# Kernel tuning notes

Measured on AMD Instinct MI355X. Metric: run time of the kernel, lower is better.

## Reference

```python
import jax, jax.numpy as jnp
import numpy as np

B, S, D = 8, 2048, 512


def setup_inputs() -> dict:
    key = jax.random.key(0)
    ks = jax.random.split(key, 8)
    x = jax.random.normal(ks[0], (B, S, D), dtype=jnp.float32)
    mask = jax.random.randint(ks[1], (B, S, 1), 0, 2, dtype=jnp.int32)
    Wq = jax.random.normal(ks[2], (D, D), dtype=jnp.float32) / np.sqrt(D)
    bq = jax.random.normal(ks[3], (D,), dtype=jnp.float32) * 0.01
    Wk = jax.random.normal(ks[4], (D, D), dtype=jnp.float32) / np.sqrt(D)
    bk = jax.random.normal(ks[5], (D,), dtype=jnp.float32) * 0.01
    Wv = jax.random.normal(ks[6], (D, D), dtype=jnp.float32) / np.sqrt(D)
    bv = jax.random.normal(ks[7], (D,), dtype=jnp.float32) * 0.01
    return {"x": x, "mask": mask, "Wq": Wq, "bq": bq, "Wk": Wk, "bk": bk, "Wv": Wv, "bv": bv}


def reference(x, mask, Wq, bq, Wk, bk, Wv, bv):
    # torch Linear: y = x @ W^T + b
    Q = jnp.einsum('bsd,ed->bse', x, Wq) + bq
    K = jnp.einsum('bsd,ed->bse', x, Wk) + bk
    V = jnp.einsum('bsd,ed->bse', x, Wv) + bv
    scale = 1.0 / jnp.sqrt(jnp.asarray(x.shape[-1], dtype=x.dtype))
    scores = jnp.einsum('bqd,bkd->bqk', Q, K) * scale  # [B, S, S]
    attn_mask = jnp.transpose(mask, (0, 2, 1))  # [B, 1, S], broadcasts over queries
    scores = jnp.where(attn_mask == 0, jnp.asarray(-10000.0, dtype=scores.dtype), scores)
    attn = jax.nn.softmax(scores, axis=-1)
    return jnp.einsum('bqk,bkd->bqd', attn, V)
```

## Files before the change

### kernel.cpp

```cpp
#include <hip/hip_runtime.h>
#include <cstddef>

#define BB 8
#define SS 2048
#define DD 512
#define MM (BB * SS)

typedef __attribute__((ext_vector_type(8))) short bf16x8;
typedef __attribute__((ext_vector_type(4))) float f32x4;
typedef __attribute__((ext_vector_type(4))) unsigned short u16x4;

__device__ __forceinline__ f32x4 mfma16(bf16x8 a, bf16x8 b, f32x4 c) {
  return __builtin_amdgcn_mfma_f32_16x16x32_bf16(a, b, c, 0, 0, 0);
}
__device__ __forceinline__ unsigned short f2bf(float f) {
  unsigned int u = __float_as_uint(f);
  u += 0x7fffu + ((u >> 16) & 1u);
  return (unsigned short)(u >> 16);
}
__device__ __forceinline__ void gld16(const void* g, void* l) {
  __builtin_amdgcn_global_load_lds((const __attribute__((address_space(1))) void*)g,
                                   (__attribute__((address_space(3))) void*)l, 16, 0, 0);
}

__global__ void cvt_bf16_kernel(const float* __restrict__ in,
                                unsigned short* __restrict__ out, int n4) {
  int i = blockIdx.x * blockDim.x + threadIdx.x;
  if (i >= n4) return;
  f32x4 v = reinterpret_cast<const f32x4*>(in)[i];
  u16x4 o;
  o[0] = f2bf(v[0]);
  o[1] = f2bf(v[1]);
  o[2] = f2bf(v[2]);
  o[3] = f2bf(v[3]);
  reinterpret_cast<u16x4*>(out)[i] = o;
}
__global__ void cvt_w3_kernel(const float* __restrict__ s0, const float* __restrict__ s1,
                              const float* __restrict__ s2, unsigned short* __restrict__ d0,
                              unsigned short* __restrict__ d1, unsigned short* __restrict__ d2) {
  const float* s = blockIdx.y == 0 ? s0 : (blockIdx.y == 1 ? s1 : s2);
  unsigned short* d = blockIdx.y == 0 ? d0 : (blockIdx.y == 1 ? d1 : d2);
  int i = blockIdx.x * blockDim.x + threadIdx.x;
  f32x4 v = reinterpret_cast<const f32x4*>(s)[i];
  u16x4 o;
  o[0] = f2bf(v[0]);
  o[1] = f2bf(v[1]);
  o[2] = f2bf(v[2]);
  o[3] = f2bf(v[3]);
  reinterpret_cast<u16x4*>(d)[i] = o;
}

__global__ void mask_scan_kernel(const int* __restrict__ mask, int* __restrict__ idx,
                                 int* __restrict__ nbArr) {
  __shared__ int part[256];
  const int b = blockIdx.x;
  const int t = threadIdx.x;
  int m[8], c = 0;
#pragma unroll
  for (int e = 0; e < 8; ++e) {
    m[e] = mask[b * SS + t * 8 + e];
    c += (m[e] != 0);
  }
  int v = c;
  part[t] = v;
  __syncthreads();
  for (int off = 1; off < 256; off <<= 1) {
    int u = (t >= off) ? part[t - off] : 0;
    __syncthreads();
    v += u;
    part[t] = v;
    __syncthreads();
  }
  int base = v - c;
#pragma unroll
  for (int e = 0; e < 8; ++e)
    if (m[e]) idx[b * SS + base++] = t * 8 + e;
  const int nb = part[255];
  if (t == 255) nbArr[b] = nb;
  for (int j = nb + t; j < SS; j += 256) idx[b * SS + j] = 0;
}

__global__ __launch_bounds__(256, 2) void qkv_gemm_kernel(
    const unsigned short* __restrict__ X, const unsigned short* __restrict__ W0,
    const unsigned short* __restrict__ W1, const unsigned short* __restrict__ W2,
    const float* __restrict__ b0, const float* __restrict__ b1,
    const float* __restrict__ b2, unsigned short* __restrict__ O0,
    unsigned short* __restrict__ O1, unsigned short* __restrict__ O2) {
  __shared__ unsigned char a_lds[128 * 128];
  __shared__ unsigned char b_lds[128 * 128];
  const int tid = threadIdx.x;
  const int w = tid >> 6, l = tid & 63, lr = l & 15, hi = l >> 4;
  const int which = blockIdx.y >> 2;
  const unsigned short* W = which == 0 ? W0 : (which == 1 ? W1 : W2);
  const float* bias = which == 0 ? b0 : (which == 1 ? b1 : b2);
  unsigned short* out = which == 0 ? O0 : (which == 1 ? O1 : O2);
  const int m0 = blockIdx.x * 128;
  const int n0 = (blockIdx.y & 3) * 128;
  const int wm = (w >> 1) * 64, wn = (w & 1) * 64;
  const int srow = l >> 3, gchunk = (l & 7) ^ (srow & 7);

  f32x4 acc[4][4];
#pragma unroll
  for (int mt = 0; mt < 4; ++mt)
#pragma unroll
    for (int nt = 0; nt < 4; ++nt) acc[mt][nt] = (f32x4){0.f, 0.f, 0.f, 0.f};

  const unsigned short* ga = X + (size_t)(m0 + w * 32 + srow) * DD + gchunk * 8;
  const unsigned short* gb = W + (size_t)(n0 + w * 32 + srow) * DD + gchunk * 8;

  for (int k0 = 0; k0 < DD; k0 += 64) {
#pragma unroll
    for (int ii = 0; ii < 4; ++ii) {
      gld16(ga + (size_t)ii * 8 * DD + k0, &a_lds[(w * 4 + ii) * 1024]);
      gld16(gb + (size_t)ii * 8 * DD + k0, &b_lds[(w * 4 + ii) * 1024]);
    }
    __syncthreads();
#pragma unroll
    for (int dkl = 0; dkl < 2; ++dkl) {
      const int gc = dkl * 4 + hi;
      bf16x8 af[4], bfr[4];
#pragma unroll
      for (int mt = 0; mt < 4; ++mt) {
        const int row = wm + mt * 16 + lr;
        af[mt] = *reinterpret_cast<const bf16x8*>(
            &a_lds[row * 128 + ((gc ^ (row & 7)) * 16)]);
      }
#pragma unroll
      for (int nt = 0; nt < 4; ++nt) {
        const int row = wn + nt * 16 + lr;
        bfr[nt] = *reinterpret_cast<const bf16x8*>(
            &b_lds[row * 128 + ((gc ^ (row & 7)) * 16)]);
      }
#pragma unroll
      for (int mt = 0; mt < 4; ++mt)
#pragma unroll
        for (int nt = 0; nt < 4; ++nt)
          acc[mt][nt] = mfma16(af[mt], bfr[nt], acc[mt][nt]);
    }
    __syncthreads();
  }

#pragma unroll
  for (int nt = 0; nt < 4; ++nt) {
    const int col = n0 + wn + nt * 16 + lr;
    const float bv = bias[col];
#pragma unroll
    for (int mt = 0; mt < 4; ++mt)
#pragma unroll
      for (int r = 0; r < 4; ++r) {
        const int row = m0 + wm + mt * 16 + hi * 4 + r;
        out[(size_t)row * DD + col] = f2bf(acc[mt][nt][r] + bv);
      }
  }
}

__global__ void vtrans_kernel(const unsigned short* __restrict__ V,
                              const int* __restrict__ idx, const int* __restrict__ nbArr,
                              unsigned short* __restrict__ VT2) {
  __shared__ unsigned short t[64][72];
  const int b = blockIdx.z;
  const int kt = blockIdx.x;
  const int d0 = blockIdx.y * 64;
  const int tid = threadIdx.x;
  const int c = tid & 63, rg = tid >> 6;
  const int nb = nbArr[b];
#pragma unroll
  for (int i = 0; i < 16; ++i) {
    const int row = rg * 16 + i;
    const int s = kt * 64 + row;
    const int src = s < nb ? idx[b * SS + s] : 0;
    t[row][c] = V[((size_t)b * SS + src) * DD + d0 + c];
  }
  __syncthreads();
#pragma unroll
  for (int i = 0; i < 16; ++i) {
    const int ix = i * 256 + tid;
    const int jj = ix & 7;
    const int dl = (ix >> 3) & 63;
    const int cc = ix >> 9;
    VT2[(((size_t)(b * 32 + kt) * 8 + cc) * 512 + d0 + dl) * 8 + jj] =
        t[cc * 8 + jj][dl];
  }
}

__global__ __launch_bounds__(256, 2) void attn_kernel(
    const unsigned short* __restrict__ Q, const unsigned short* __restrict__ K,
    const unsigned short* __restrict__ VT2, const int* __restrict__ idx,
    const int* __restrict__ nbArr, float* __restrict__ Out,
    float* __restrict__ Apart, float* __restrict__ mlpart) {
  __shared__ unsigned char k_lds[32 * 1024];
  __shared__ unsigned char vt_lds[4 * 512 * 16];
  __shared__ unsigned short pbuf[4][16][32];
  const int tid = threadIdx.x;
  const int w = tid >> 6, l = tid & 63, lr = l & 15, hi = l >> 4;
  const int bid = blockIdx.x;
  const int b = bid & 7;
  const int qt = (bid >> 3) >> 1;
  const int sp = (bid >> 3) & 1;
  const int q0 = qt * 64 + w * 16;
  const float scale = 0.044194173824159216f;

  const int nb = nbArr[b];
  const int ntile = (nb + 31) >> 5;
  const int half = (ntile + 1) >> 1;
  const int lo = sp == 0 ? 0 : half;
  const int hi_t = sp == 0 ? half : ntile;

  const unsigned short* __restrict__ Qb = Q + (size_t)b * SS * DD;
  const unsigned short* __restrict__ Kb = K + (size_t)b * SS * DD;
  const unsigned short* __restrict__ Vb = VT2 + (size_t)b * SS * DD;
  const int* __restrict__ idxb = idx + b * SS;

  bf16x8 qf[16];
#pragma unroll
  for (int dk = 0; dk < 16; ++dk)
    qf[dk] = *reinterpret_cast<const bf16x8*>(
        &Qb[(size_t)(q0 + lr) * DD + dk * 32 + hi * 8]);

  f32x4 oacc[32];
#pragma unroll
  for (int i = 0; i < 32; ++i) oacc[i] = (f32x4){0.f, 0.f, 0.f, 0.f};
  float mrow[4], lrow[4];
#pragma unroll
  for (int r = 0; r < 4; ++r) {
    mrow[r] = -10000.0f;
    lrow[r] = 0.0f;
  }

  for (int t = lo; t < hi_t; ++t) {
#pragma unroll
    for (int r = 0; r < 8; ++r) {
      const int row = w * 8 + r;
      const int j = t * 32 + row;
      const int src = idxb[j];
      const int ch = (l & 56) | ((l ^ row) & 7);
      gld16(Kb + (size_t)src * DD + ch * 8, &k_lds[row * 1024]);
    }
    const size_t vbase = ((size_t)((t >> 1) * 8 + (t & 1) * 4 + w) * 512);
#pragma unroll
    for (int g = 0; g < 8; ++g)
      gld16(Vb + (vbase + g * 64 + l) * 8, &vt_lds[(w * 512 + g * 64) * 16]);
    __syncthreads();

    f32x4 sacc[2];
#pragma unroll
    for (int nt = 0; nt < 2; ++nt) sacc[nt] = (f32x4){0.f, 0.f, 0.f, 0.f};
#pragma unroll
    for (int dk = 0; dk < 16; ++dk) {
#pragma unroll
      for (int nt = 0; nt < 2; ++nt) {
        const int row = nt * 16 + lr;
        const int c = dk * 4 + hi;
        bf16x8 bk = *reinterpret_cast<const bf16x8*>(
            &k_lds[row * 1024 + ((c & ~7) | ((c ^ row) & 7)) * 16]);
        sacc[nt] = mfma16(qf[dk], bk, sacc[nt]);
      }
    }

    float s[2][4];
#pragma unroll
    for (int nt = 0; nt < 2; ++nt) {
      const int j = t * 32 + nt * 16 + lr;
      const bool ok = j < nb;
#pragma unroll
      for (int r = 0; r < 4; ++r)
        s[nt][r] = ok ? sacc[nt][r] * scale : -10000.0f;
    }

    float mnew[4], alpha[4];
#pragma unroll
    for (int r = 0; r < 4; ++r) {
      float mx = fmaxf(s[0][r], s[1][r]);
#pragma unroll
      for (int off = 1; off < 16; off <<= 1) mx = fmaxf(mx, __shfl_xor(mx, off));
      mnew[r] = fmaxf(mrow[r], mx);
      alpha[r] = __expf(mrow[r] - mnew[r]);
      mrow[r] = mnew[r];
    }
    float rs[4] = {0.f, 0.f, 0.f, 0.f};
#pragma unroll
    for (int nt = 0; nt < 2; ++nt)
#pragma unroll
      for (int r = 0; r < 4; ++r) {
        float p = __expf(s[nt][r] - mnew[r]);
        s[nt][r] = p;
        rs[r] += p;
      }
#pragma unroll
    for (int r = 0; r < 4; ++r) {
      float tt = rs[r];
#pragma unroll
      for (int off = 1; off < 16; off <<= 1) tt += __shfl_xor(tt, off);
      lrow[r] = lrow[r] * alpha[r] + tt;
    }

#pragma unroll
    for (int nt = 0; nt < 2; ++nt)
#pragma unroll
      for (int r = 0; r < 4; ++r)
        pbuf[w][hi * 4 + r][nt * 16 + lr] = f2bf(s[nt][r]);
    bf16x8 pf = *reinterpret_cast<const bf16x8*>(&pbuf[w][lr][hi * 8]);

    const float aprod = alpha[0] * alpha[1] * alpha[2] * alpha[3];
    unsigned long long bal = __ballot(aprod == 1.0f);
    if (bal != ~0ull) {
#pragma unroll
      for (int nt2 = 0; nt2 < 32; ++nt2)
#pragma unroll
        for (int r = 0; r < 4; ++r) oacc[nt2][r] *= alpha[r];
    }
#pragma unroll
    for (int nt2 = 0; nt2 < 32; ++nt2) {
      bf16x8 v0 = *reinterpret_cast<const bf16x8*>(
          &vt_lds[(hi * 512 + nt2 * 16 + lr) * 16]);
      oacc[nt2] = mfma16(pf, v0, oacc[nt2]);
    }
    __syncthreads();
  }

  float* Ap = sp == 0 ? Out : Apart;
#pragma unroll
  for (int nt2 = 0; nt2 < 32; ++nt2)
#pragma unroll
    for (int r = 0; r < 4; ++r)
      Ap[((size_t)b * SS + q0 + hi * 4 + r) * DD + nt2 * 16 + lr] = oacc[nt2][r];
  if (lr == 0) {
#pragma unroll
    for (int r = 0; r < 4; ++r) {
      const size_t row = (size_t)sp * MM + b * SS + q0 + hi * 4 + r;
      mlpart[row * 2 + 0] = mrow[r];
      mlpart[row * 2 + 1] = lrow[r];
    }
  }
}

__global__ void combine_kernel(float* __restrict__ Out, const float* __restrict__ Apart,
                               const float* __restrict__ mlpart) {
  const int gid = blockIdx.x * 256 + threadIdx.x;
  const int row = gid >> 7;
  const float m1 = mlpart[(size_t)row * 2 + 0];
  const float l1 = mlpart[(size_t)row * 2 + 1];
  const float m2 = mlpart[((size_t)MM + row) * 2 + 0];
  const float l2 = mlpart[((size_t)MM + row) * 2 + 1];
  const float m = fmaxf(m1, m2);
  const float w1 = __expf(m1 - m), w2 = __expf(m2 - m);
  const float inv = 1.0f / (w1 * l1 + w2 * l2);
  f32x4 a1 = reinterpret_cast<f32x4*>(Out)[gid];
  f32x4 a2 = reinterpret_cast<const f32x4*>(Apart)[gid];
  f32x4 o;
#pragma unroll
  for (int e = 0; e < 4; ++e) o[e] = (w1 * a1[e] + w2 * a2[e]) * inv;
  reinterpret_cast<f32x4*>(Out)[gid] = o;
}

extern "C" void kernel_launch(void* const* d_in, const int* in_sizes, int n_in,
                              void* d_out, int out_size, void* d_ws, size_t ws_size,
                              hipStream_t stream) {
  const float* x = (const float*)d_in[0];
  const int* mask = (const int*)d_in[1];
  const float* Wq = (const float*)d_in[2];
  const float* bq = (const float*)d_in[3];
  const float* Wk = (const float*)d_in[4];
  const float* bk = (const float*)d_in[5];
  const float* Wv = (const float*)d_in[6];
  const float* bv = (const float*)d_in[7];
  float* out = (float*)d_out;

  char* ws = (char*)d_ws;
  const size_t MB = 1024 * 1024;
  unsigned short* Qb = (unsigned short*)(ws);
  unsigned short* Kb = (unsigned short*)(ws + 16 * MB);
  unsigned short* VT2b = (unsigned short*)(ws + 32 * MB);
  unsigned short* Xb = (unsigned short*)(ws + 48 * MB);
  unsigned short* Vb = (unsigned short*)(ws + 64 * MB);
  float* Apart = (float*)(ws + 48 * MB);
  unsigned short* Wqb = (unsigned short*)(ws + 80 * MB);
  unsigned short* Wkb = Wqb + 512 * 512;
  unsigned short* Wvb = Wkb + 512 * 512;
  int* idx = (int*)(ws + 82 * MB);
  int* nbArr = (int*)(ws + 82 * MB + 65536);
  float* mlpart = (float*)(ws + 82 * MB + 128 * 1024);

  cvt_bf16_kernel<<<8192, 256, 0, stream>>>(x, Xb, (MM * DD) / 4);
  cvt_w3_kernel<<<dim3(256, 3), 256, 0, stream>>>(Wq, Wk, Wv, Wqb, Wkb, Wvb);
  mask_scan_kernel<<<BB, 256, 0, stream>>>(mask, idx, nbArr);

  qkv_gemm_kernel<<<dim3(MM / 128, 12), 256, 0, stream>>>(
      Xb, Wqb, Wkb, Wvb, bq, bk, bv, Qb, Kb, Vb);

  vtrans_kernel<<<dim3(SS / 64, DD / 64, BB), 256, 0, stream>>>(Vb, idx, nbArr, VT2b);

  attn_kernel<<<512, 256, 0, stream>>>(Qb, Kb, VT2b, idx, nbArr, out, Apart, mlpart);

  combine_kernel<<<(MM * DD / 4) / 256, 256, 0, stream>>>(out, Apart, mlpart);
}
```

Baseline: 252.1 us.

## Compact unmasked keys before K/V projection and restructure attention PV loop

Unmasked key rows of x are scattered into a compacted buffer during the bf16 conversion. K and V are then projected only for valid key tiles, skipping masked-out rows, and the V transpose skips empty tiles. The attention kernel drops the idx gather, prefetches the next K/V tile between barriers, and shares P and alpha across waves through LDS so each wave computes a 128-column slice for all 64 queries. Weight conversion and the mask scan are merged into one launch. This adds scatter writes and extra LDS traffic and barriers, and the saving depends on how much of the mask is zero.

```diff
diff --git a/kernel.cpp b/kernel.cpp
--- a/kernel.cpp
+++ b/kernel.cpp
@@ -23,38 +23,26 @@
                                    (__attribute__((address_space(3))) void*)l, 16, 0, 0);
 }
 
-__global__ void cvt_bf16_kernel(const float* __restrict__ in,
-                                unsigned short* __restrict__ out, int n4) {
-  int i = blockIdx.x * blockDim.x + threadIdx.x;
-  if (i >= n4) return;
-  f32x4 v = reinterpret_cast<const f32x4*>(in)[i];
-  u16x4 o;
-  o[0] = f2bf(v[0]);
-  o[1] = f2bf(v[1]);
-  o[2] = f2bf(v[2]);
-  o[3] = f2bf(v[3]);
-  reinterpret_cast<u16x4*>(out)[i] = o;
-}
-__global__ void cvt_w3_kernel(const float* __restrict__ s0, const float* __restrict__ s1,
-                              const float* __restrict__ s2, unsigned short* __restrict__ d0,
-                              unsigned short* __restrict__ d1, unsigned short* __restrict__ d2) {
-  const float* s = blockIdx.y == 0 ? s0 : (blockIdx.y == 1 ? s1 : s2);
-  unsigned short* d = blockIdx.y == 0 ? d0 : (blockIdx.y == 1 ? d1 : d2);
-  int i = blockIdx.x * blockDim.x + threadIdx.x;
-  f32x4 v = reinterpret_cast<const f32x4*>(s)[i];
-  u16x4 o;
-  o[0] = f2bf(v[0]);
-  o[1] = f2bf(v[1]);
-  o[2] = f2bf(v[2]);
-  o[3] = f2bf(v[3]);
-  reinterpret_cast<u16x4*>(d)[i] = o;
-}
-
-__global__ void mask_scan_kernel(const int* __restrict__ mask, int* __restrict__ idx,
-                                 int* __restrict__ nbArr) {
+__global__ void prep_kernel(const float* __restrict__ Wq, const float* __restrict__ Wk,
+                            const float* __restrict__ Wv, unsigned short* __restrict__ Wqb,
+                            unsigned short* __restrict__ Wkb, unsigned short* __restrict__ Wvb,
+                            const int* __restrict__ mask, int* __restrict__ posArr,
+                            int* __restrict__ nbArr) {
   __shared__ int part[256];
-  const int b = blockIdx.x;
+  const int bx = blockIdx.x;
   const int t = threadIdx.x;
+  if (bx < 768) {
+    const int which = bx >> 8;
+    const float* s = which == 0 ? Wq : (which == 1 ? Wk : Wv);
+    unsigned short* d = which == 0 ? Wqb : (which == 1 ? Wkb : Wvb);
+    const int i = (bx & 255) * 256 + t;
+    f32x4 v = reinterpret_cast<const f32x4*>(s)[i];
+    u16x4 o;
+    o[0] = f2bf(v[0]); o[1] = f2bf(v[1]); o[2] = f2bf(v[2]); o[3] = f2bf(v[3]);
+    reinterpret_cast<u16x4*>(d)[i] = o;
+    return;
+  }
+  const int b = bx - 768;
   int m[8], c = 0;
 #pragma unroll
   for (int e = 0; e < 8; ++e) {
@@ -73,29 +61,54 @@
   }
   int base = v - c;
 #pragma unroll
-  for (int e = 0; e < 8; ++e)
-    if (m[e]) idx[b * SS + base++] = t * 8 + e;
-  const int nb = part[255];
-  if (t == 255) nbArr[b] = nb;
-  for (int j = nb + t; j < SS; j += 256) idx[b * SS + j] = 0;
+  for (int e = 0; e < 8; ++e) {
+    posArr[b * SS + t * 8 + e] = m[e] ? base : -1;
+    if (m[e]) ++base;
+  }
+  if (t == 255) nbArr[b] = part[255];
+}
+
+__global__ void cvtx_kernel(const float* __restrict__ x, const int* __restrict__ posArr,
+                            unsigned short* __restrict__ Xb, unsigned short* __restrict__ Xc) {
+  const int gid = blockIdx.x * 256 + threadIdx.x;
+  const int col4 = gid & 127;
+  const int row = gid >> 7;
+  f32x4 v = reinterpret_cast<const f32x4*>(x)[gid];
+  u16x4 o;
+  o[0] = f2bf(v[0]); o[1] = f2bf(v[1]); o[2] = f2bf(v[2]); o[3] = f2bf(v[3]);
+  reinterpret_cast<u16x4*>(Xb)[gid] = o;
+  const int p = posArr[row];
+  if (p >= 0) {
+    const int b = row >> 11;
+    reinterpret_cast<u16x4*>(Xc)[((size_t)(b << 11) + p) * 128 + col4] = o;
+  }
 }
 
 __global__ __launch_bounds__(256, 2) void qkv_gemm_kernel(
-    const unsigned short* __restrict__ X, const unsigned short* __restrict__ W0,
-    const unsigned short* __restrict__ W1, const unsigned short* __restrict__ W2,
-    const float* __restrict__ b0, const float* __restrict__ b1,
-    const float* __restrict__ b2, unsigned short* __restrict__ O0,
-    unsigned short* __restrict__ O1, unsigned short* __restrict__ O2) {
+    const unsigned short* __restrict__ Xb, const unsigned short* __restrict__ Xc,
+    const unsigned short* __restrict__ W0, const unsigned short* __restrict__ W1,
+    const unsigned short* __restrict__ W2, const float* __restrict__ b0,
+    const float* __restrict__ b1, const float* __restrict__ b2,
+    unsigned short* __restrict__ Qb, unsigned short* __restrict__ Kc,
+    unsigned short* __restrict__ Vc, const int* __restrict__ nbArr) {
   __shared__ unsigned char a_lds[128 * 128];
   __shared__ unsigned char b_lds[128 * 128];
+  const int which = blockIdx.z;
+  int m0;
+  const unsigned short* X;
+  unsigned short* out;
+  if (which == 0) {
+    X = Xb; out = Qb; m0 = blockIdx.x * 128;
+  } else {
+    const int b = blockIdx.x >> 4, mt0 = blockIdx.x & 15;
+    if (mt0 * 128 >= nbArr[b]) return;
+    X = Xc; out = (which == 1) ? Kc : Vc; m0 = b * SS + mt0 * 128;
+  }
+  const unsigned short* W = which == 0 ? W0 : (which == 1 ? W1 : W2);
+  const float* bias = which == 0 ? b0 : (which == 1 ? b1 : b2);
   const int tid = threadIdx.x;
   const int w = tid >> 6, l = tid & 63, lr = l & 15, hi = l >> 4;
-  const int which = blockIdx.y >> 2;
-  const unsigned short* W = which == 0 ? W0 : (which == 1 ? W1 : W2);
-  const float* bias = which == 0 ? b0 : (which == 1 ? b1 : b2);
-  unsigned short* out = which == 0 ? O0 : (which == 1 ? O1 : O2);
-  const int m0 = blockIdx.x * 128;
-  const int n0 = (blockIdx.y & 3) * 128;
+  const int n0 = blockIdx.y * 128;
   const int wm = (w >> 1) * 64, wn = (w & 1) * 64;
   const int srow = l >> 3, gchunk = (l & 7) ^ (srow & 7);
 
@@ -154,22 +167,22 @@
   }
 }
 
-__global__ void vtrans_kernel(const unsigned short* __restrict__ V,
-                              const int* __restrict__ idx, const int* __restrict__ nbArr,
+__global__ void vtrans_kernel(const unsigned short* __restrict__ Vc,
+                              const int* __restrict__ nbArr,
                               unsigned short* __restrict__ VT2) {
   __shared__ unsigned short t[64][72];
   const int b = blockIdx.z;
   const int kt = blockIdx.x;
+  const int nb = nbArr[b];
+  if (kt * 64 >= nb) return;
   const int d0 = blockIdx.y * 64;
   const int tid = threadIdx.x;
   const int c = tid & 63, rg = tid >> 6;
-  const int nb = nbArr[b];
 #pragma unroll
   for (int i = 0; i < 16; ++i) {
     const int row = rg * 16 + i;
     const int s = kt * 64 + row;
-    const int src = s < nb ? idx[b * SS + s] : 0;
-    t[row][c] = V[((size_t)b * SS + src) * DD + d0 + c];
+    t[row][c] = (s < nb) ? Vc[((size_t)b * SS + s) * DD + d0 + c] : (unsigned short)0;
   }
   __syncthreads();
 #pragma unroll
@@ -184,13 +197,13 @@
 }
 
 __global__ __launch_bounds__(256, 2) void attn_kernel(
-    const unsigned short* __restrict__ Q, const unsigned short* __restrict__ K,
-    const unsigned short* __restrict__ VT2, const int* __restrict__ idx,
-    const int* __restrict__ nbArr, float* __restrict__ Out,
-    float* __restrict__ Apart, float* __restrict__ mlpart) {
+    const unsigned short* __restrict__ Q, const unsigned short* __restrict__ Kc,
+    const unsigned short* __restrict__ VT2, const int* __restrict__ nbArr,
+    float* __restrict__ Out, float* __restrict__ Apart, float* __restrict__ mlpart) {
   __shared__ unsigned char k_lds[32 * 1024];
   __shared__ unsigned char vt_lds[4 * 512 * 16];
   __shared__ unsigned short pbuf[4][16][32];
+  __shared__ __align__(16) float alds[68];
   const int tid = threadIdx.x;
   const int w = tid >> 6, l = tid & 63, lr = l & 15, hi = l >> 4;
   const int bid = blockIdx.x;
@@ -207,9 +220,8 @@
   const int hi_t = sp == 0 ? half : ntile;
 
   const unsigned short* __restrict__ Qb = Q + (size_t)b * SS * DD;
-  const unsigned short* __restrict__ Kb = K + (size_t)b * SS * DD;
+  const unsigned short* __restrict__ Kb = Kc + (size_t)b * SS * DD;
   const unsigned short* __restrict__ Vb = VT2 + (size_t)b * SS * DD;
-  const int* __restrict__ idxb = idx + b * SS;
 
   bf16x8 qf[16];
 #pragma unroll
@@ -227,19 +239,24 @@
     lrow[r] = 0.0f;
   }
 
-  for (int t = lo; t < hi_t; ++t) {
+  auto stageK = [&](int t) {
 #pragma unroll
     for (int r = 0; r < 8; ++r) {
       const int row = w * 8 + r;
-      const int j = t * 32 + row;
-      const int src = idxb[j];
       const int ch = (l & 56) | ((l ^ row) & 7);
-      gld16(Kb + (size_t)src * DD + ch * 8, &k_lds[row * 1024]);
-    }
+      gld16(Kb + (size_t)(t * 32 + row) * DD + ch * 8, &k_lds[row * 1024]);
+    }
+  };
+  auto stageV = [&](int t) {
     const size_t vbase = ((size_t)((t >> 1) * 8 + (t & 1) * 4 + w) * 512);
 #pragma unroll
     for (int g = 0; g < 8; ++g)
       gld16(Vb + (vbase + g * 64 + l) * 8, &vt_lds[(w * 512 + g * 64) * 16]);
+  };
+
+  if (lo < hi_t) { stageK(lo); stageV(lo); }
+
+  for (int t = lo; t < hi_t; ++t) {
     __syncthreads();
 
     f32x4 sacc[2];
@@ -256,7 +273,6 @@
         sacc[nt] = mfma16(qf[dk], bk, sacc[nt]);
       }
     }
-
     float s[2][4];
 #pragma unroll
     for (int nt = 0; nt < 2; ++nt) {
@@ -266,7 +282,6 @@
       for (int r = 0; r < 4; ++r)
         s[nt][r] = ok ? sacc[nt][r] * scale : -10000.0f;
     }
-
     float mnew[4], alpha[4];
 #pragma unroll
     for (int r = 0; r < 4; ++r) {
@@ -293,37 +308,58 @@
       for (int off = 1; off < 16; off <<= 1) tt += __shfl_xor(tt, off);
       lrow[r] = lrow[r] * alpha[r] + tt;
     }
-
 #pragma unroll
     for (int nt = 0; nt < 2; ++nt)
 #pragma unroll
       for (int r = 0; r < 4; ++r)
         pbuf[w][hi * 4 + r][nt * 16 + lr] = f2bf(s[nt][r]);
-    bf16x8 pf = *reinterpret_cast<const bf16x8*>(&pbuf[w][lr][hi * 8]);
-
+    if (lr == 0)
+      *reinterpret_cast<f32x4*>(&alds[w * 16 + hi * 4]) =
+          (f32x4){alpha[0], alpha[1], alpha[2], alpha[3]};
     const float aprod = alpha[0] * alpha[1] * alpha[2] * alpha[3];
     unsigned long long bal = __ballot(aprod == 1.0f);
-    if (bal != ~0ull) {
-#pragma unroll
-      for (int nt2 = 0; nt2 < 32; ++nt2)
-#pragma unroll
-        for (int r = 0; r < 4; ++r) oacc[nt2][r] *= alpha[r];
-    }
-#pragma unroll
-    for (int nt2 = 0; nt2 < 32; ++nt2) {
-      bf16x8 v0 = *reinterpret_cast<const bf16x8*>(
-          &vt_lds[(hi * 512 + nt2 * 16 + lr) * 16]);
-      oacc[nt2] = mfma16(pf, v0, oacc[nt2]);
-    }
-    __syncthreads();
+    if (l == 0) alds[64 + w] = (bal == ~0ull) ? 1.0f : 0.0f;
+
+    __syncthreads();
+    if (t + 1 < hi_t) stageK(t + 1);
+
+    f32x4 fl = *reinterpret_cast<const f32x4*>(&alds[64]);
+    bf16x8 af[4];
+#pragma unroll
+    for (int mt = 0; mt < 4; ++mt)
+      af[mt] = *reinterpret_cast<const bf16x8*>(&pbuf[mt][lr][hi * 8]);
+    if (fl[0] + fl[1] + fl[2] + fl[3] < 4.0f) {
+#pragma unroll
+      for (int mt = 0; mt < 4; ++mt) {
+        f32x4 al = *reinterpret_cast<const f32x4*>(&alds[mt * 16 + hi * 4]);
+#pragma unroll
+        for (int nt = 0; nt < 8; ++nt)
+#pragma unroll
+          for (int r = 0; r < 4; ++r) oacc[mt * 8 + nt][r] *= al[r];
+      }
+    }
+#pragma unroll
+    for (int nt = 0; nt < 8; ++nt) {
+      bf16x8 bv = *reinterpret_cast<const bf16x8*>(
+          &vt_lds[(hi * 512 + w * 128 + nt * 16 + lr) * 16]);
+#pragma unroll
+      for (int mt = 0; mt < 4; ++mt)
+        oacc[mt * 8 + nt] = mfma16(af[mt], bv, oacc[mt * 8 + nt]);
+    }
+
+    __syncthreads();
+    if (t + 1 < hi_t) stageV(t + 1);
   }
 
   float* Ap = sp == 0 ? Out : Apart;
 #pragma unroll
-  for (int nt2 = 0; nt2 < 32; ++nt2)
-#pragma unroll
-    for (int r = 0; r < 4; ++r)
-      Ap[((size_t)b * SS + q0 + hi * 4 + r) * DD + nt2 * 16 + lr] = oacc[nt2][r];
+  for (int mt = 0; mt < 4; ++mt)
+#pragma unroll
+    for (int nt = 0; nt < 8; ++nt)
+#pragma unroll
+      for (int r = 0; r < 4; ++r)
+        Ap[((size_t)b * SS + qt * 64 + mt * 16 + hi * 4 + r) * DD + w * 128 +
+           nt * 16 + lr] = oacc[mt * 8 + nt][r];
   if (lr == 0) {
 #pragma unroll
     for (int r = 0; r < 4; ++r) {
@@ -369,28 +405,24 @@
   char* ws = (char*)d_ws;
   const size_t MB = 1024 * 1024;
   unsigned short* Qb = (unsigned short*)(ws);
-  unsigned short* Kb = (unsigned short*)(ws + 16 * MB);
+  unsigned short* Kc = (unsigned short*)(ws + 16 * MB);
+  unsigned short* Xc = (unsigned short*)(ws + 32 * MB);
   unsigned short* VT2b = (unsigned short*)(ws + 32 * MB);
   unsigned short* Xb = (unsigned short*)(ws + 48 * MB);
-  unsigned short* Vb = (unsigned short*)(ws + 64 * MB);
+  unsigned short* Vc = (unsigned short*)(ws + 64 * MB);
   float* Apart = (float*)(ws + 48 * MB);
   unsigned short* Wqb = (unsigned short*)(ws + 80 * MB);
   unsigned short* Wkb = Wqb + 512 * 512;
   unsigned short* Wvb = Wkb + 512 * 512;
-  int* idx = (int*)(ws + 82 * MB);
+  int* posArr = (int*)(ws + 82 * MB);
   int* nbArr = (int*)(ws + 82 * MB + 65536);
   float* mlpart = (float*)(ws + 82 * MB + 128 * 1024);
 
-  cvt_bf16_kernel<<<8192, 256, 0, stream>>>(x, Xb, (MM * DD) / 4);
-  cvt_w3_kernel<<<dim3(256, 3), 256, 0, stream>>>(Wq, Wk, Wv, Wqb, Wkb, Wvb);
-  mask_scan_kernel<<<BB, 256, 0, stream>>>(mask, idx, nbArr);
-
-  qkv_gemm_kernel<<<dim3(MM / 128, 12), 256, 0, stream>>>(
-      Xb, Wqb, Wkb, Wvb, bq, bk, bv, Qb, Kb, Vb);
-
-  vtrans_kernel<<<dim3(SS / 64, DD / 64, BB), 256, 0, stream>>>(Vb, idx, nbArr, VT2b);
-
-  attn_kernel<<<512, 256, 0, stream>>>(Qb, Kb, VT2b, idx, nbArr, out, Apart, mlpart);
-
-  combine_kernel<<<(MM * DD / 4) / 256, 256, 0, stream>>>(out, Apart, mlpart);
-}
+  prep_kernel<<<776, 256, 0, stream>>>(Wq, Wk, Wv, Wqb, Wkb, Wvb, mask, posArr, nbArr);
+  cvtx_kernel<<<8192, 256, 0, stream>>>(x, posArr, Xb, Xc);
+  qkv_gemm_kernel<<<dim3(128, 4, 3), 256, 0, stream>>>(
+      Xb, Xc, Wqb, Wkb, Wvb, bq, bk, bv, Qb, Kc, Vc, nbArr);
+  vtrans_kernel<<<dim3(32, 8, 8), 256, 0, stream>>>(Vc, nbArr, VT2b);
+  attn_kernel<<<512, 256, 0, stream>>>(Qb, Kc, VT2b, nbArr, out, Apart, mlpart);
+  combine_kernel<<<8192, 256, 0, stream>>>(out, Apart, mlpart);
+}
```

Result: no change. 253.4 us (+0.5%).
